# Optimization experiments

Measured on AMD Instinct MI355X. Metric: run time of the kernel, lower is better.

The kernel has to match this reference:

```python
import jax, jax.numpy as jnp
import numpy as np

jax.config.update("jax_enable_x64", True)

# Dims (see shape_source): batch, heads, q-len, kv-len, head-channels, quant group
B, H, T, S, HC = 2, 16, 1024, 1024, 128
G = 8            # group_size from A/R_QUANT_PARAMS
SCALE_SHIFT = 14 # combined dequant shift applied to integer QK scores before softmax
O_SM = 14        # fixed-point offset of the integer softmax output (LUT-style)
PROB_QMAX = 255.0  # 8-bit unsigned probability mantissa (R_QUANT_PARAMS n_bits=8)


def _dequant_po2(q, s):
    """q: int mantissas [..., N], s: nonneg po2 shift exponents [..., N//G].
    Emulates (q << s) per group of G channels (pot_scale activation quantizer)."""
    s_full = jnp.repeat(s, G, axis=-1)
    return q.astype(jnp.float64) * jnp.exp2(s_full.astype(jnp.float64))


def setup_inputs() -> dict:
    key = jax.random.key(0)
    ks = jax.random.split(key, 6)
    # signed 8-bit mantissas in [-128, 127]
    q_q = jax.random.randint(ks[0], (B, H, T, HC), 0, 256, dtype=jnp.int32) - 128
    k_q = jax.random.randint(ks[1], (B, H, S, HC), 0, 256, dtype=jnp.int32) - 128
    vt_q = jax.random.randint(ks[2], (B, H, HC, S), 0, 256, dtype=jnp.int32) - 128
    # nonnegative power-of-two shifts, one per group of G=8
    q_s = jax.random.randint(ks[3], (B, H, T, HC // G), 0, 4, dtype=jnp.int32)
    k_s = jax.random.randint(ks[4], (B, H, S, HC // G), 0, 4, dtype=jnp.int32)
    vt_s = jax.random.randint(ks[5], (B, H, HC, S // G), 0, 4, dtype=jnp.int32)
    return {"q_q": q_q, "q_s": q_s, "k_q": k_q, "k_s": k_s, "vt_q": vt_q, "vt_s": vt_s}


def reference(q_q, q_s, k_q, k_s, vt_q, vt_s):
    # ---- shift_qk_matmul: (q_q << q_s) @ (k_q << k_s)^T in float64, truncated to int64
    q = _dequant_po2(q_q, q_s)                       # [B,H,T,HC] f64
    k = _dequant_po2(k_q, k_s)                       # [B,H,S,HC] f64
    scores = jnp.einsum("bhtc,bhsc->bhts", q, k).astype(jnp.int64)

    # ---- integer softmax emulation: rescale integer scores, softmax, then
    # re-quantize probabilities with an 8-bit per-group (G=8 along S) po2 scale
    logits = scores.astype(jnp.float32) * np.float32(2.0 ** (-SCALE_SHIFT) / np.sqrt(HC))
    p = jax.nn.softmax(logits, axis=-1)              # [B,H,T,S]
    val = jnp.round(p * (2.0 ** O_SM))               # fixed-point probs (ints)
    vg = val.reshape(B, H, T, S // G, G)
    gmax = jnp.max(vg, axis=-1, keepdims=True)
    r_shift = jnp.clip(jnp.ceil(jnp.log2(jnp.maximum(gmax, 1.0) / PROB_QMAX)), 0.0, None)
    r_q = jnp.clip(jnp.round(vg / jnp.exp2(r_shift)), 0.0, PROB_QMAX)
    r = (r_q * jnp.exp2(r_shift)).reshape(B, H, T, S).astype(jnp.float64)  # (r_q << r_s)

    # ---- shift_rv_matmul: r @ (vt_q << vt_s)^T in float64, truncated to int64
    vt = _dequant_po2(vt_q, vt_s)                    # [B,H,HC,S] f64
    a = jnp.einsum("bhts,bhcs->bhtc", r, vt).astype(jnp.int64)  # [B,H,T,HC]
    return a
```

## Files before the change

kernel.cpp:

```cpp
#include <hip/hip_runtime.h>
#include <string.h>


typedef int   v4i __attribute__((ext_vector_type(4)));
typedef float v4f __attribute__((ext_vector_type(4)));
typedef short v8s __attribute__((ext_vector_type(8)));
typedef unsigned v2u __attribute__((ext_vector_type(2)));

#define BHN 32
#define TN  1024
#define SN  1024
#define HCN 128
#define TT  16
#define RST 1032
#define KD_BH 262144
#define VD_BH 262144
#define WS_NEED ((size_t)BHN*(KD_BH+VD_BH))

__device__ __forceinline__ unsigned pack_b(int b0,int b1,int b2,int b3){
    return (unsigned)((b0&255)|((b1&255)<<8)|((b2&255)<<16)|((b3&255)<<24));
}

__device__ __forceinline__ void dig16(const int* __restrict__ p, int s0, int s1,
                                      v4i& hi, v4i& lo){
    #pragma unroll
    for (int wi=0; wi<4; ++wi){
        v4i m = *(const v4i*)(p + wi*4);
        int s = (wi<2) ? s0 : s1;
        int d0=m[0]<<s, d1=m[1]<<s, d2=m[2]<<s, d3=m[3]<<s;
        hi[wi] = (int)pack_b(d0>>4,d1>>4,d2>>4,d3>>4);
        lo[wi] = (int)pack_b(d0&15,d1&15,d2&15,d3&15);
    }
}

__device__ __forceinline__ unsigned short bf16_of_int(int v){
    return (unsigned short)(__float_as_uint((float)v) >> 16);
}

__global__ __launch_bounds__(256) void digitize(
    const int* __restrict__ k_q, const int* __restrict__ k_s,
    const int* __restrict__ vt_q, const int* __restrict__ vt_s,
    unsigned char* __restrict__ kd, unsigned char* __restrict__ vd)
{
    const int w    = threadIdx.x >> 6;
    const int lane = threadIdx.x & 63;
    const int l15  = lane & 15;
    const int task = blockIdx.x*4 + w;
    if (task < 4096){
        const int kc = task & 1, n = (task>>1)&7, ch = (task>>4)&7, bh = task>>7;
        const int q4   = lane >> 4;
        const int srow = bh*SN + ch*128 + n*16 + l15;
        const int gb   = srow*16 + kc*8 + q4*2;
        v4i hi, lo;
        dig16(k_q + (size_t)srow*HCN + kc*64 + q4*16, k_s[gb], k_s[gb+1], hi, lo);
        size_t base = (size_t)bh*KD_BH + (size_t)(ch*32768 + n*4096 + kc*2048 + lane*16);
        *(v4i*)(kd + base)        = hi;
        *(v4i*)(kd + base + 1024) = lo;
    } else {
        const int t  = task - 4096;
        const int n  = t & 7, kb = (t>>3)&31, bh = t>>8;
        const int sub = lane >> 4;
        const int row = bh*HCN + n*16 + l15;
        const int* vp = vt_q + (size_t)row*SN + kb*32 + sub*8;
        const int s   = vt_s[row*128 + kb*4 + sub];
        unsigned wds[4];
        #pragma unroll
        for (int j=0;j<4;j++){
            int a = vp[j*2]   << s;
            int b = vp[j*2+1] << s;
            wds[j] = (unsigned)bf16_of_int(a) | ((unsigned)bf16_of_int(b) << 16);
        }
        size_t base = (size_t)bh*VD_BH + (size_t)(((kb*8 + n)*64 + lane)*16);
        *(v4i*)(vd + base) = v4i{(int)wds[0],(int)wds[1],(int)wds[2],(int)wds[3]};
    }
}

template<bool PK>
__global__ __launch_bounds__(256,4) void mha_mfma(
    const int* __restrict__ q_q, const int* __restrict__ q_s,
    const int* __restrict__ k_q, const int* __restrict__ k_s,
    const int* __restrict__ vt_q, const int* __restrict__ vt_s,
    const unsigned char* __restrict__ kd, const unsigned char* __restrict__ vd,
    int* __restrict__ out)
{
    __shared__ __align__(16) unsigned short rbuf[16*RST];
    __shared__ float red[128];

    const int tid  = threadIdx.x;
    const int ln   = tid & 15;
    const int qd4  = (tid >> 4) & 3;
    const int w    = tid >> 6;
    const int lane = tid & 63;
    const int blk = blockIdx.x;
    const int bh  = ((blk>>9)<<3) | (blk&7);
    const int t0  = ((blk>>3)&63) * TT;

    v4i qfh[2], qfl[2];
    {
        const int* qrow  = q_q + (size_t)(bh*TN + t0 + ln)*HCN;
        const int* qsrow = q_s + (size_t)(bh*TN + t0 + ln)*16;
        #pragma unroll
        for (int kc=0; kc<2; ++kc){
            int gi = kc*8 + qd4*2;
            dig16(qrow + kc*64 + qd4*16, qsrow[gi], qsrow[gi+1], qfh[kc], qfl[kc]);
        }
    }

    int scv[16][4];

    const v4i* kb_ = (const v4i*)(kd + (size_t)bh*KD_BH);
    for (int ch=0; ch<8; ++ch){
        #pragma unroll
        for (int i=0;i<2;i++){
            const int n = w*2 + i;
            v4i a2{0,0,0,0}, a1{0,0,0,0}, a0{0,0,0,0};
            #pragma unroll
            for (int kc=0;kc<2;kc++){
                v4i bhv, blv;
                if (PK){
                    const v4i* tb = kb_ + (ch*8+n)*256 + kc*128 + lane;
                    bhv = tb[0];
                    blv = tb[64];
                } else {
                    int srow = bh*SN + ch*128 + n*16 + ln;
                    int cc   = kc*64 + qd4*16;
                    dig16(k_q + (size_t)srow*128 + cc,
                          k_s[srow*16 + (cc>>3)], k_s[srow*16 + (cc>>3) + 1], bhv, blv);
                }
                a2 = __builtin_amdgcn_mfma_i32_16x16x64_i8(bhv, qfh[kc], a2, 0,0,0);
                a1 = __builtin_amdgcn_mfma_i32_16x16x64_i8(bhv, qfl[kc], a1, 0,0,0);
                a1 = __builtin_amdgcn_mfma_i32_16x16x64_i8(blv, qfh[kc], a1, 0,0,0);
                a0 = __builtin_amdgcn_mfma_i32_16x16x64_i8(blv, qfl[kc], a0, 0,0,0);
            }
            int st = ch*2 + i;
            #pragma unroll
            for (int r=0;r<4;r++)
                scv[st][r] = (a2[r]<<8) + (a1[r]<<4) + a0[r];
        }
    }

    const float CS2 = (float)(6.103515625e-05 / 11.313708498984760390566
                              * 1.4426950408889634074);
    {
        float m0=-3.0e38f, m1=-3.0e38f, m2=-3.0e38f, m3=-3.0e38f;
        #pragma unroll
        for (int st=0;st<16;st++){
            float f0 = (float)scv[st][0]*CS2; scv[st][0]=__float_as_int(f0); m0=fmaxf(m0,f0);
            float f1 = (float)scv[st][1]*CS2; scv[st][1]=__float_as_int(f1); m1=fmaxf(m1,f1);
            float f2 = (float)scv[st][2]*CS2; scv[st][2]=__float_as_int(f2); m2=fmaxf(m2,f2);
            float f3 = (float)scv[st][3]*CS2; scv[st][3]=__float_as_int(f3); m3=fmaxf(m3,f3);
        }
        float m_ = fmaxf(fmaxf(m0,m1), fmaxf(m2,m3));
        m_ = fmaxf(m_, __shfl_xor(m_, 16));
        m_ = fmaxf(m_, __shfl_xor(m_, 32));
        if ((tid & 48) == 0) red[w*16 + ln] = m_;
    }
    __syncthreads();
    const float mrow = fmaxf(fmaxf(red[ln], red[16+ln]), fmaxf(red[32+ln], red[48+ln]));
    float inv14;
    {
        float s0=0.f, s1=0.f, s2=0.f, s3=0.f;
        #pragma unroll
        for (int st=0;st<16;st++){
            #pragma unroll
            for (int r=0;r<4;r++){
                float t_ = __int_as_float(scv[st][r]) - mrow;
                float e;
                asm("v_exp_f32 %0, %1" : "=v"(e) : "v"(t_));
                scv[st][r] = __float_as_int(e);
                if (r==0) s0 += e; else if (r==1) s1 += e; else if (r==2) s2 += e; else s3 += e;
            }
        }
        float s_ = (s0+s1) + (s2+s3);
        s_ += __shfl_xor(s_, 16);
        s_ += __shfl_xor(s_, 32);
        if ((tid & 48) == 0) red[64 + w*16 + ln] = s_;
    }
    __syncthreads();
    {
        float sum = red[64+ln] + red[80+ln] + red[96+ln] + red[112+ln];
        inv14 = 16384.0f / sum;
    }

    {
        unsigned short* rp = rbuf + ln*RST;
        const int swzr = (ln & 7) ^ ((ln & 8) >> 1);
        const int cbase = (w*2)*16 + qd4*4;
        #pragma unroll
        for (int st=0;st<16;st++){
            float v0 = rintf(__int_as_float(scv[st][0]) * inv14);
            float v1 = rintf(__int_as_float(scv[st][1]) * inv14);
            float v2 = rintf(__int_as_float(scv[st][2]) * inv14);
            float v3 = rintf(__int_as_float(scv[st][3]) * inv14);
            float g = fmaxf(fmaxf(v0,v1), fmaxf(v2,v3));
            g = fmaxf(g, __shfl_xor(g, 16));
            int gi = max((int)g, 1);
            int x  = gi - 1;
            int e2 = 31 - __clz(x | 255);
            int sh = (e2 - 7) + ((x >> (e2 - 7)) == 255);
            float isc = __int_as_float((127 - sh) << 23);
            float fsc = __int_as_float((127 + sh) << 23);
            unsigned b0 = __float_as_uint(rintf(v0*isc) * fsc);
            unsigned b1 = __float_as_uint(rintf(v1*isc) * fsc);
            unsigned b2 = __float_as_uint(rintf(v2*isc) * fsc);
            unsigned b3 = __float_as_uint(rintf(v3*isc) * fsc);
            unsigned w0 = __builtin_amdgcn_perm(b1, b0, 0x07060302u);
            unsigned w1 = __builtin_amdgcn_perm(b3, b2, 0x07060302u);
            int c0 = ((st>>1)*128) + cbase + ((st&1)*16);
            int gs = (c0>>3) ^ swzr;
            *(v2u*)(rp + gs*8 + (c0&7)) = v2u{w0, w1};
        }
    }
    __syncthreads();

    const v4i* vb = (const v4i*)(vd + (size_t)bh*VD_BH);
    const unsigned short* rp2 = rbuf + ln*RST;
    const int swzr2 = (ln & 7) ^ ((ln & 8) >> 1);
    v4f acc0{0,0,0,0}, acc1{0,0,0,0};
    #pragma unroll 4
    for (int kb=0; kb<32; ++kb){
        v8s af = *(const v8s*)(rp2 + (((kb*4+qd4) ^ swzr2) << 3));
        v4i b0, b1;
        if (PK){
            b0 = vb[(kb*8 + w*2    )*64 + lane];
            b1 = vb[(kb*8 + w*2 + 1)*64 + lane];
        } else {
            #pragma unroll
            for (int i=0;i<2;i++){
                int chan = (w*2+i)*16 + ln;
                const int* vp = vt_q + (size_t)(bh*HCN + chan)*SN + kb*32 + qd4*8;
                int s = vt_s[(bh*HCN + chan)*128 + kb*4 + qd4];
                unsigned wd[4];
                #pragma unroll
                for (int j=0;j<4;j++){
                    int a = vp[j*2]   << s;
                    int b = vp[j*2+1] << s;
                    wd[j] = (unsigned)bf16_of_int(a) | ((unsigned)bf16_of_int(b)<<16);
                }
                v4i t{(int)wd[0],(int)wd[1],(int)wd[2],(int)wd[3]};
                if (i==0) b0 = t; else b1 = t;
            }
        }
        v8s bs0, bs1;
        memcpy(&bs0, &b0, 16);
        memcpy(&bs1, &b1, 16);
        acc0 = __builtin_amdgcn_mfma_f32_16x16x32_bf16(af, bs0, acc0, 0,0,0);
        acc1 = __builtin_amdgcn_mfma_f32_16x16x32_bf16(af, bs1, acc1, 0,0,0);
    }
    #pragma unroll
    for (int r=0;r<4;r++){
        size_t o = (size_t)(bh*TN + t0 + qd4*4 + r)*HCN + (w*2)*16 + ln;
        out[o]      = (int)rintf(acc0[r]);
        out[o + 16] = (int)rintf(acc1[r]);
    }
}

extern "C" void kernel_launch(void* const* d_in, const int* in_sizes, int n_in,
                              void* d_out, int out_size, void* d_ws, size_t ws_size,
                              hipStream_t stream) {
    const int* q_q  = (const int*)d_in[0];
    const int* q_s  = (const int*)d_in[1];
    const int* k_q  = (const int*)d_in[2];
    const int* k_s  = (const int*)d_in[3];
    const int* vt_q = (const int*)d_in[4];
    const int* vt_s = (const int*)d_in[5];
    int* out = (int*)d_out;

    unsigned char* kd = (unsigned char*)d_ws;
    unsigned char* vd = kd + (size_t)BHN*KD_BH;

    if (ws_size >= WS_NEED){
        digitize<<<dim3(3072), 256, 0, stream>>>(k_q,k_s,vt_q,vt_s, kd,vd);
        mha_mfma<true><<<dim3(2048), 256, 0, stream>>>(
            q_q,q_s,k_q,k_s,vt_q,vt_s, kd,vd, out);
    } else {
        mha_mfma<false><<<dim3(2048), 256, 0, stream>>>(
            q_q,q_s,k_q,k_s,vt_q,vt_s, kd,vd, out);
    }
}
```

Baseline: 151.8 us.

## Process 32 query rows per block to reuse K/V fragments across two tiles

Each block now handles two 16-row query tiles instead of one, so every loaded K and V fragment feeds twice as many MFMAs, and the grid shrinks to 1024 blocks. The LDS probability buffer doubles to 64KB and its swizzle changes from XOR to a rotate-style pattern without row padding. Register pressure roughly doubles (scores for 32 rows are held in registers), so launch bounds drop to 2 blocks per CU, trading occupancy for reuse. The ch loop is also fully unrolled.

```diff
diff --git a/kernel.cpp b/kernel.cpp
--- a/kernel.cpp
+++ b/kernel.cpp
@@ -11,8 +11,7 @@
 #define TN  1024
 #define SN  1024
 #define HCN 128
-#define TT  16
-#define RST 1032
+#define TT  32
 #define KD_BH 262144
 #define VD_BH 262144
 #define WS_NEED ((size_t)BHN*(KD_BH+VD_BH))
@@ -76,15 +75,15 @@
 }
 
 template<bool PK>
-__global__ __launch_bounds__(256,4) void mha_mfma(
+__global__ __launch_bounds__(256,2) void mha_mfma(
     const int* __restrict__ q_q, const int* __restrict__ q_s,
     const int* __restrict__ k_q, const int* __restrict__ k_s,
     const int* __restrict__ vt_q, const int* __restrict__ vt_s,
     const unsigned char* __restrict__ kd, const unsigned char* __restrict__ vd,
     int* __restrict__ out)
 {
-    __shared__ __align__(16) unsigned short rbuf[16*RST];
-    __shared__ float red[128];
+    __shared__ __align__(16) unsigned short rbuf[32*1024];
+    __shared__ float red[256];
 
     const int tid  = threadIdx.x;
     const int ln   = tid & 15;
@@ -92,28 +91,31 @@
     const int w    = tid >> 6;
     const int lane = tid & 63;
     const int blk = blockIdx.x;
-    const int bh  = ((blk>>9)<<3) | (blk&7);
-    const int t0  = ((blk>>3)&63) * TT;
-
-    v4i qfh[2], qfl[2];
-    {
-        const int* qrow  = q_q + (size_t)(bh*TN + t0 + ln)*HCN;
-        const int* qsrow = q_s + (size_t)(bh*TN + t0 + ln)*16;
+    const int bh  = ((blk>>8)<<3) | (blk&7);
+    const int t0  = ((blk>>3)&31) * TT;
+
+    v4i qfh[2][2], qfl[2][2];
+    #pragma unroll
+    for (int h=0; h<2; ++h){
+        const int* qrow  = q_q + (size_t)(bh*TN + t0 + h*16 + ln)*HCN;
+        const int* qsrow = q_s + (size_t)(bh*TN + t0 + h*16 + ln)*16;
         #pragma unroll
         for (int kc=0; kc<2; ++kc){
             int gi = kc*8 + qd4*2;
-            dig16(qrow + kc*64 + qd4*16, qsrow[gi], qsrow[gi+1], qfh[kc], qfl[kc]);
-        }
-    }
-
-    int scv[16][4];
+            dig16(qrow + kc*64 + qd4*16, qsrow[gi], qsrow[gi+1], qfh[h][kc], qfl[h][kc]);
+        }
+    }
+
+    int scv[2][16][4];
 
     const v4i* kb_ = (const v4i*)(kd + (size_t)bh*KD_BH);
+    #pragma unroll
     for (int ch=0; ch<8; ++ch){
         #pragma unroll
         for (int i=0;i<2;i++){
             const int n = w*2 + i;
-            v4i a2{0,0,0,0}, a1{0,0,0,0}, a0{0,0,0,0};
+            v4i a2[2]={{0,0,0,0},{0,0,0,0}}, a1[2]={{0,0,0,0},{0,0,0,0}},
+                a0[2]={{0,0,0,0},{0,0,0,0}};
             #pragma unroll
             for (int kc=0;kc<2;kc++){
                 v4i bhv, blv;
@@ -127,99 +129,117 @@
                     dig16(k_q + (size_t)srow*128 + cc,
                           k_s[srow*16 + (cc>>3)], k_s[srow*16 + (cc>>3) + 1], bhv, blv);
                 }
-                a2 = __builtin_amdgcn_mfma_i32_16x16x64_i8(bhv, qfh[kc], a2, 0,0,0);
-                a1 = __builtin_amdgcn_mfma_i32_16x16x64_i8(bhv, qfl[kc], a1, 0,0,0);
-                a1 = __builtin_amdgcn_mfma_i32_16x16x64_i8(blv, qfh[kc], a1, 0,0,0);
-                a0 = __builtin_amdgcn_mfma_i32_16x16x64_i8(blv, qfl[kc], a0, 0,0,0);
+                #pragma unroll
+                for (int h=0;h<2;h++){
+                    a2[h] = __builtin_amdgcn_mfma_i32_16x16x64_i8(bhv, qfh[h][kc], a2[h], 0,0,0);
+                    a1[h] = __builtin_amdgcn_mfma_i32_16x16x64_i8(bhv, qfl[h][kc], a1[h], 0,0,0);
+                    a1[h] = __builtin_amdgcn_mfma_i32_16x16x64_i8(blv, qfh[h][kc], a1[h], 0,0,0);
+                    a0[h] = __builtin_amdgcn_mfma_i32_16x16x64_i8(blv, qfl[h][kc], a0[h], 0,0,0);
+                }
             }
             int st = ch*2 + i;
             #pragma unroll
-            for (int r=0;r<4;r++)
-                scv[st][r] = (a2[r]<<8) + (a1[r]<<4) + a0[r];
+            for (int h=0;h<2;h++)
+                #pragma unroll
+                for (int r=0;r<4;r++)
+                    scv[h][st][r] = (a2[h][r]<<8) + (a1[h][r]<<4) + a0[h][r];
         }
     }
 
     const float CS2 = (float)(6.103515625e-05 / 11.313708498984760390566
                               * 1.4426950408889634074);
-    {
+    #pragma unroll
+    for (int h=0;h<2;h++){
         float m0=-3.0e38f, m1=-3.0e38f, m2=-3.0e38f, m3=-3.0e38f;
         #pragma unroll
         for (int st=0;st<16;st++){
-            float f0 = (float)scv[st][0]*CS2; scv[st][0]=__float_as_int(f0); m0=fmaxf(m0,f0);
-            float f1 = (float)scv[st][1]*CS2; scv[st][1]=__float_as_int(f1); m1=fmaxf(m1,f1);
-            float f2 = (float)scv[st][2]*CS2; scv[st][2]=__float_as_int(f2); m2=fmaxf(m2,f2);
-            float f3 = (float)scv[st][3]*CS2; scv[st][3]=__float_as_int(f3); m3=fmaxf(m3,f3);
+            float f0 = (float)scv[h][st][0]*CS2; scv[h][st][0]=__float_as_int(f0); m0=fmaxf(m0,f0);
+            float f1 = (float)scv[h][st][1]*CS2; scv[h][st][1]=__float_as_int(f1); m1=fmaxf(m1,f1);
+            float f2 = (float)scv[h][st][2]*CS2; scv[h][st][2]=__float_as_int(f2); m2=fmaxf(m2,f2);
+            float f3 = (float)scv[h][st][3]*CS2; scv[h][st][3]=__float_as_int(f3); m3=fmaxf(m3,f3);
         }
         float m_ = fmaxf(fmaxf(m0,m1), fmaxf(m2,m3));
         m_ = fmaxf(m_, __shfl_xor(m_, 16));
         m_ = fmaxf(m_, __shfl_xor(m_, 32));
-        if ((tid & 48) == 0) red[w*16 + ln] = m_;
+        if ((tid & 48) == 0) red[h*64 + w*16 + ln] = m_;
     }
     __syncthreads();
-    const float mrow = fmaxf(fmaxf(red[ln], red[16+ln]), fmaxf(red[32+ln], red[48+ln]));
-    float inv14;
-    {
+    float inv14[2];
+    #pragma unroll
+    for (int h=0;h<2;h++){
+        const float mrow = fmaxf(fmaxf(red[h*64+ln], red[h*64+16+ln]),
+                                 fmaxf(red[h*64+32+ln], red[h*64+48+ln]));
         float s0=0.f, s1=0.f, s2=0.f, s3=0.f;
         #pragma unroll
         for (int st=0;st<16;st++){
             #pragma unroll
             for (int r=0;r<4;r++){
-                float t_ = __int_as_float(scv[st][r]) - mrow;
+                float t_ = __int_as_float(scv[h][st][r]) - mrow;
                 float e;
                 asm("v_exp_f32 %0, %1" : "=v"(e) : "v"(t_));
-                scv[st][r] = __float_as_int(e);
+                scv[h][st][r] = __float_as_int(e);
                 if (r==0) s0 += e; else if (r==1) s1 += e; else if (r==2) s2 += e; else s3 += e;
             }
         }
         float s_ = (s0+s1) + (s2+s3);
         s_ += __shfl_xor(s_, 16);
         s_ += __shfl_xor(s_, 32);
-        if ((tid & 48) == 0) red[64 + w*16 + ln] = s_;
+        if ((tid & 48) == 0) red[128 + h*64 + w*16 + ln] = s_;
     }
     __syncthreads();
+    #pragma unroll
+    for (int h=0;h<2;h++){
+        float sum = red[128+h*64+ln] + red[128+h*64+16+ln]
+                  + red[128+h*64+32+ln] + red[128+h*64+48+ln];
+        inv14[h] = 16384.0f / sum;
+    }
+
     {
-        float sum = red[64+ln] + red[80+ln] + red[96+ln] + red[112+ln];
-        inv14 = 16384.0f / sum;
-    }
-
-    {
-        unsigned short* rp = rbuf + ln*RST;
-        const int swzr = (ln & 7) ^ ((ln & 8) >> 1);
-        const int cbase = (w*2)*16 + qd4*4;
-        #pragma unroll
-        for (int st=0;st<16;st++){
-            float v0 = rintf(__int_as_float(scv[st][0]) * inv14);
-            float v1 = rintf(__int_as_float(scv[st][1]) * inv14);
-            float v2 = rintf(__int_as_float(scv[st][2]) * inv14);
-            float v3 = rintf(__int_as_float(scv[st][3]) * inv14);
-            float g = fmaxf(fmaxf(v0,v1), fmaxf(v2,v3));
-            g = fmaxf(g, __shfl_xor(g, 16));
-            int gi = max((int)g, 1);
-            int x  = gi - 1;
-            int e2 = 31 - __clz(x | 255);
-            int sh = (e2 - 7) + ((x >> (e2 - 7)) == 255);
-            float isc = __int_as_float((127 - sh) << 23);
-            float fsc = __int_as_float((127 + sh) << 23);
-            unsigned b0 = __float_as_uint(rintf(v0*isc) * fsc);
-            unsigned b1 = __float_as_uint(rintf(v1*isc) * fsc);
-            unsigned b2 = __float_as_uint(rintf(v2*isc) * fsc);
-            unsigned b3 = __float_as_uint(rintf(v3*isc) * fsc);
-            unsigned w0 = __builtin_amdgcn_perm(b1, b0, 0x07060302u);
-            unsigned w1 = __builtin_amdgcn_perm(b3, b2, 0x07060302u);
-            int c0 = ((st>>1)*128) + cbase + ((st&1)*16);
-            int gs = (c0>>3) ^ swzr;
-            *(v2u*)(rp + gs*8 + (c0&7)) = v2u{w0, w1};
+        const int lnr = ln & 7;
+        const int cbase = w*32 + qd4*4;
+        #pragma unroll
+        for (int h=0;h<2;h++){
+            unsigned short* rp = rbuf + (h*16 + ln)*1024;
+            #pragma unroll
+            for (int st=0;st<16;st++){
+                float v0 = rintf(__int_as_float(scv[h][st][0]) * inv14[h]);
+                float v1 = rintf(__int_as_float(scv[h][st][1]) * inv14[h]);
+                float v2 = rintf(__int_as_float(scv[h][st][2]) * inv14[h]);
+                float v3 = rintf(__int_as_float(scv[h][st][3]) * inv14[h]);
+                float g = fmaxf(fmaxf(v0,v1), fmaxf(v2,v3));
+                g = fmaxf(g, __shfl_xor(g, 16));
+                int gi = max((int)g, 1);
+                int x  = gi - 1;
+                int e2 = 31 - __clz(x | 255);
+                int sh = (e2 - 7) + ((x >> (e2 - 7)) == 255);
+                float isc = __int_as_float((127 - sh) << 23);
+                float fsc = __int_as_float((127 + sh) << 23);
+                unsigned b0 = __float_as_uint(rintf(v0*isc) * fsc);
+                unsigned b1 = __float_as_uint(rintf(v1*isc) * fsc);
+                unsigned b2 = __float_as_uint(rintf(v2*isc) * fsc);
+                unsigned b3 = __float_as_uint(rintf(v3*isc) * fsc);
+                unsigned w0 = __builtin_amdgcn_perm(b1, b0, 0x07060302u);
+                unsigned w1 = __builtin_amdgcn_perm(b3, b2, 0x07060302u);
+                int c0 = (st>>1)*128 + cbase + (st&1)*16;
+                int g_ = c0 >> 3;
+                int gs = (g_ & 0x78) | ((g_ + lnr) & 7);
+                *(v2u*)(rp + gs*8 + (c0&7)) = v2u{w0, w1};
+            }
         }
     }
     __syncthreads();
 
     const v4i* vb = (const v4i*)(vd + (size_t)bh*VD_BH);
-    const unsigned short* rp2 = rbuf + ln*RST;
-    const int swzr2 = (ln & 7) ^ ((ln & 8) >> 1);
-    v4f acc0{0,0,0,0}, acc1{0,0,0,0};
+    const unsigned short* rp0 = rbuf + ln*1024;
+    const unsigned short* rp1 = rbuf + (16 + ln)*1024;
+    const int lnr2 = ln & 7;
+    v4f acc00{0,0,0,0}, acc01{0,0,0,0}, acc10{0,0,0,0}, acc11{0,0,0,0};
     #pragma unroll 4
     for (int kb=0; kb<32; ++kb){
-        v8s af = *(const v8s*)(rp2 + (((kb*4+qd4) ^ swzr2) << 3));
+        int g2  = kb*4 + qd4;
+        int gs2 = (g2 & 0x78) | ((g2 + lnr2) & 7);
+        v8s af0 = *(const v8s*)(rp0 + gs2*8);
+        v8s af1 = *(const v8s*)(rp1 + gs2*8);
         v4i b0, b1;
         if (PK){
             b0 = vb[(kb*8 + w*2    )*64 + lane];
@@ -244,14 +264,19 @@
         v8s bs0, bs1;
         memcpy(&bs0, &b0, 16);
         memcpy(&bs1, &b1, 16);
-        acc0 = __builtin_amdgcn_mfma_f32_16x16x32_bf16(af, bs0, acc0, 0,0,0);
-        acc1 = __builtin_amdgcn_mfma_f32_16x16x32_bf16(af, bs1, acc1, 0,0,0);
+        acc00 = __builtin_amdgcn_mfma_f32_16x16x32_bf16(af0, bs0, acc00, 0,0,0);
+        acc01 = __builtin_amdgcn_mfma_f32_16x16x32_bf16(af0, bs1, acc01, 0,0,0);
+        acc10 = __builtin_amdgcn_mfma_f32_16x16x32_bf16(af1, bs0, acc10, 0,0,0);
+        acc11 = __builtin_amdgcn_mfma_f32_16x16x32_bf16(af1, bs1, acc11, 0,0,0);
     }
     #pragma unroll
     for (int r=0;r<4;r++){
-        size_t o = (size_t)(bh*TN + t0 + qd4*4 + r)*HCN + (w*2)*16 + ln;
-        out[o]      = (int)rintf(acc0[r]);
-        out[o + 16] = (int)rintf(acc1[r]);
+        size_t o0 = (size_t)(bh*TN + t0 + qd4*4 + r)*HCN + w*32 + ln;
+        out[o0]      = (int)rintf(acc00[r]);
+        out[o0 + 16] = (int)rintf(acc01[r]);
+        size_t o1 = o0 + (size_t)16*HCN;
+        out[o1]      = (int)rintf(acc10[r]);
+        out[o1 + 16] = (int)rintf(acc11[r]);
     }
 }
 
@@ -271,10 +296,10 @@
 
     if (ws_size >= WS_NEED){
         digitize<<<dim3(3072), 256, 0, stream>>>(k_q,k_s,vt_q,vt_s, kd,vd);
-        mha_mfma<true><<<dim3(2048), 256, 0, stream>>>(
+        mha_mfma<true><<<dim3(1024), 256, 0, stream>>>(
             q_q,q_s,k_q,k_s,vt_q,vt_s, kd,vd, out);
     } else {
-        mha_mfma<false><<<dim3(2048), 256, 0, stream>>>(
+        mha_mfma<false><<<dim3(1024), 256, 0, stream>>>(
             q_q,q_s,k_q,k_s,vt_q,vt_s, kd,vd, out);
     }
 }
```

Result: slower. 176.8 us (+16.5%).
